# Optimization experiments

Hardware: AMD Instinct MI355X
Metric: run time of the kernel (lower is better)

## Reference

```python
import jax, jax.numpy as jnp
import numpy as np

DIM = 1024
FF = 4096
BATCH = 4
SEQ = 2048
EPS = 1e-5


def setup_inputs() -> dict:
    key = jax.random.key(0)
    ks = jax.random.split(key, 8)
    x = jax.random.normal(ks[0], (BATCH, SEQ, DIM), dtype=jnp.float32)
    # phazor init: exp(2j*pi*arange(dim)/dim) * |randn(dim)|
    ang = 2.0 * np.pi * jnp.arange(DIM, dtype=jnp.float32) / DIM
    mag = jnp.abs(jax.random.normal(ks[1], (DIM,), dtype=jnp.float32))
    phazor_re = mag * jnp.cos(ang)
    phazor_im = mag * jnp.sin(ang)
    last_re = jax.random.normal(ks[2], (DIM,), dtype=jnp.float32)
    last_im = jax.random.normal(ks[3], (DIM,), dtype=jnp.float32)
    w1 = jax.random.normal(ks[4], (FF, DIM), dtype=jnp.float32) * DIM ** -0.5
    b1 = jnp.zeros((FF,), dtype=jnp.float32)
    w2 = jax.random.normal(ks[5], (DIM, FF), dtype=jnp.float32) * FF ** -0.5
    b2 = jnp.zeros((DIM,), dtype=jnp.float32)
    return {
        'x': x,
        'ln1_w': jnp.ones((DIM,), jnp.float32), 'ln1_b': jnp.zeros((DIM,), jnp.float32),
        'ln2_w': jnp.ones((DIM,), jnp.float32), 'ln2_b': jnp.zeros((DIM,), jnp.float32),
        'sc_lin': jnp.ones((DIM,), jnp.float32),
        'phazor_re': phazor_re, 'phazor_im': phazor_im,
        'last_re': last_re, 'last_im': last_im,
        'w1': w1, 'b1': b1, 'w2': w2, 'b2': b2,
    }


def _layer_norm(x, w, b):
    mu = jnp.mean(x, axis=-1, keepdims=True)
    var = jnp.mean(jnp.square(x - mu), axis=-1, keepdims=True)
    return (x - mu) * jax.lax.rsqrt(var + EPS) * w + b


def _sconv(x, phazor_re, phazor_im, last_re, last_im):
    B, L, D = x.shape
    dtype = x.dtype
    xc = x.astype(jnp.complex64)
    p_raw = phazor_re + 1j * phazor_im
    # tanh(|p|) * exp(i*angle(p))
    p = (jnp.tanh(jnp.abs(p_raw)) * jnp.exp(1j * jnp.angle(p_raw))).astype(jnp.complex64)
    t = jnp.arange(L)[:, None]
    prog = jnp.power(p[None, :], t)            # [L, D] complex
    filt_fft = jnp.fft.fft(prog, n=2 * L, axis=0)   # [2L, D]
    x_fft = jnp.fft.fft(xc, n=2 * L, axis=1)        # [B, 2L, D]
    conv = jnp.fft.ifft(filt_fft[None] * x_fft, axis=1)[:, :L]  # [B, L, D]
    last = (last_re + 1j * last_im)[None, None, :]  # [1,1,D] broadcast over batch
    conv_with_past = conv + last * prog[None] * p[None, None]
    return conv_with_past.real.astype(dtype)


def reference(x, ln1_w, ln1_b, ln2_w, ln2_b, sc_lin,
              phazor_re, phazor_im, last_re, last_im,
              w1, b1, w2, b2):
    # SConv branch
    x_res = x
    h = _layer_norm(x, ln1_w, ln1_b)
    h = jax.nn.silu(h)
    h = _sconv(h, phazor_re, phazor_im, last_re, last_im)
    h = h * sc_lin
    x = h + x_res
    # FFN branch
    x_res = x
    h = _layer_norm(x, ln2_w, ln2_b)
    h = jax.nn.silu(jnp.einsum('bld,fd->blf', h, w1) + b1)
    h = jnp.einsum('blf,df->bld', h, w2) + b2
    return h + x_res
```

## Files before the change

kernel.cpp:

```cpp
#include <hip/hip_runtime.h>
#include <cmath>


#define DIMD 1024
#define FFD  4096
#define BATCH 4
#define SEQL 2048
#define MROWS (BATCH*SEQL)
#define EPSF 1e-5f
#define CHUNKS 128
#define CLEN (SEQL/CHUNKS)

typedef __attribute__((ext_vector_type(8))) _Float16 half8;
typedef __attribute__((ext_vector_type(4))) _Float16 half4;
typedef __attribute__((ext_vector_type(4))) float    floatx4;

#define E_OFF    0u
#define SV_OFF   4194304u
#define H2_OFF   8388608u
#define W1H_OFF  25165824u
#define W2H_OFF  33554432u
#define Y1_OFF   41943040u

__device__ __forceinline__ void load_lds16(const _Float16* g, _Float16* l) {
    __builtin_amdgcn_global_load_lds(
        (const __attribute__((address_space(1))) unsigned int*)g,
        (__attribute__((address_space(3))) unsigned int*)l,
        16, 0, 0);
}

__device__ __forceinline__ void wave_reduce2(float& s, float& q) {
    #pragma unroll
    for (int off = 32; off; off >>= 1) {
        s += __shfl_down(s, off, 64);
        q += __shfl_down(q, off, 64);
    }
}

__device__ __forceinline__ void get_p(const float* pre, const float* pim, int d,
                                      float& pr, float& pi) {
    float re = pre[d], im = pim[d];
    float r = sqrtf(re * re + im * im);
    float t = tanhf(r) / fmaxf(r, 1e-30f);
    pr = re * t; pi = im * t;
}

__global__ __launch_bounds__(256)
void cast2_f32_f16(const float* __restrict__ w1, const float* __restrict__ w2,
                   _Float16* __restrict__ o1, _Float16* __restrict__ o2) {
    int i = (blockIdx.x * 256 + threadIdx.x) * 4;
    const float* src = w1;
    _Float16* dst = o1;
    if (i >= FFD * DIMD) { i -= FFD * DIMD; src = w2; dst = o2; }
    float4 v = *(const float4*)(src + i);
    half4 o;
    o.x = (_Float16)v.x; o.y = (_Float16)v.y; o.z = (_Float16)v.z; o.w = (_Float16)v.w;
    *(half4*)(dst + i) = o;
}

__global__ __launch_bounds__(256)
void scan_phase1(const float* __restrict__ x, const float* __restrict__ lw,
                 const float* __restrict__ lb, const float* __restrict__ pre,
                 const float* __restrict__ pim, float2* __restrict__ e) {
    const int tid = threadIdx.x;
    const int d0 = tid * 4;
    const int c = blockIdx.x, bb = blockIdx.y;
    const int lane = tid & 63, wave = tid >> 6;
    __shared__ float2 red[2][4];

    float pr[4], pi[4], sr[4] = {}, si[4] = {};
    #pragma unroll
    for (int q = 0; q < 4; ++q) get_p(pre, pim, d0 + q, pr[q], pi[q]);
    const float4 wv = *(const float4*)(lw + d0);
    const float4 bv = *(const float4*)(lb + d0);
    const size_t rowbase = ((size_t)bb * SEQL + (size_t)c * CLEN) * DIMD;

    for (int j = 0; j < CLEN; ++j) {
        float4 v = *(const float4*)(x + rowbase + (size_t)j * DIMD + d0);
        float s = (v.x + v.y) + (v.z + v.w);
        float q2 = (v.x * v.x + v.y * v.y) + (v.z * v.z + v.w * v.w);
        wave_reduce2(s, q2);
        if (lane == 0) red[j & 1][wave] = make_float2(s, q2);
        __syncthreads();
        float2 r0 = red[j & 1][0], r1 = red[j & 1][1];
        float2 r2 = red[j & 1][2], r3 = red[j & 1][3];
        s = (r0.x + r1.x) + (r2.x + r3.x);
        q2 = (r0.y + r1.y) + (r2.y + r3.y);
        const float mu = s * (1.f / DIMD);
        const float rs = rsqrtf(q2 * (1.f / DIMD) - mu * mu + EPSF);
        float o[4] = {
            (v.x - mu) * rs * wv.x + bv.x, (v.y - mu) * rs * wv.y + bv.y,
            (v.z - mu) * rs * wv.z + bv.z, (v.w - mu) * rs * wv.w + bv.w };
        #pragma unroll
        for (int q = 0; q < 4; ++q) {
            float hv = o[q] / (1.f + __expf(-o[q]));
            float nr = pr[q] * sr[q] - pi[q] * si[q] + hv;
            float ni = pr[q] * si[q] + pi[q] * sr[q];
            sr[q] = nr; si[q] = ni;
        }
    }
    float2* ep = e + ((size_t)bb * CHUNKS + c) * DIMD + d0;
    #pragma unroll
    for (int q = 0; q < 4; ++q) ep[q] = make_float2(sr[q], si[q]);
}

__global__ __launch_bounds__(256)
void scan_combine(const float2* __restrict__ e, const float* __restrict__ pre,
                  const float* __restrict__ pim, const float* __restrict__ lre,
                  const float* __restrict__ lim, float2* __restrict__ sv) {
    const int d = blockIdx.x * 256 + threadIdx.x;
    const int bb = blockIdx.y;
    float pr, pi; get_p(pre, pim, d, pr, pi);
    float qr = pr, qi = pi;
    #pragma unroll
    for (int s = 0; s < 4; ++s) {
        float nr = qr * qr - qi * qi;
        float ni = 2.f * qr * qi;
        qr = nr; qi = ni;
    }
    float sr = lre[d], si = lim[d];
    #pragma unroll 4
    for (int c = 0; c < CHUNKS; ++c) {
        const size_t idx = ((size_t)bb * CHUNKS + c) * DIMD + d;
        sv[idx] = make_float2(sr, si);
        float2 ec = e[idx];
        float nr = qr * sr - qi * si + ec.x;
        float ni = qr * si + qi * sr + ec.y;
        sr = nr; si = ni;
    }
}

__global__ __launch_bounds__(256)
void scan_phase2(const float* __restrict__ x, const float* __restrict__ l1w,
                 const float* __restrict__ l1b, const float* __restrict__ l2w,
                 const float* __restrict__ l2b, const float* __restrict__ pre,
                 const float* __restrict__ pim, const float* __restrict__ sc,
                 const float2* __restrict__ sv, float* __restrict__ x2,
                 _Float16* __restrict__ h2) {
    const int tid = threadIdx.x;
    const int d0 = tid * 4;
    const int c = blockIdx.x, bb = blockIdx.y;
    const int lane = tid & 63, wave = tid >> 6;
    __shared__ float2 redA[2][4];
    __shared__ float2 redB[2][4];

    float pr[4], pi[4], sr[4], si[4];
    #pragma unroll
    for (int q = 0; q < 4; ++q) {
        get_p(pre, pim, d0 + q, pr[q], pi[q]);
        float2 s0 = sv[((size_t)bb * CHUNKS + c) * DIMD + d0 + q];
        sr[q] = s0.x; si[q] = s0.y;
    }
    const float4 w1v = *(const float4*)(l1w + d0);
    const float4 b1v = *(const float4*)(l1b + d0);
    const float4 w2v = *(const float4*)(l2w + d0);
    const float4 b2v = *(const float4*)(l2b + d0);
    const float4 scv = *(const float4*)(sc + d0);
    const size_t rowbase = ((size_t)bb * SEQL + (size_t)c * CLEN) * DIMD;

    for (int j = 0; j < CLEN; ++j) {
        float4 v = *(const float4*)(x + rowbase + (size_t)j * DIMD + d0);
        float s = (v.x + v.y) + (v.z + v.w);
        float q2 = (v.x * v.x + v.y * v.y) + (v.z * v.z + v.w * v.w);
        wave_reduce2(s, q2);
        if (lane == 0) redA[j & 1][wave] = make_float2(s, q2);
        __syncthreads();
        {
            float2 r0 = redA[j & 1][0], r1 = redA[j & 1][1];
            float2 r2 = redA[j & 1][2], r3 = redA[j & 1][3];
            s = (r0.x + r1.x) + (r2.x + r3.x);
            q2 = (r0.y + r1.y) + (r2.y + r3.y);
        }
        const float mu = s * (1.f / DIMD);
        const float rs = rsqrtf(q2 * (1.f / DIMD) - mu * mu + EPSF);
        float o[4] = {
            (v.x - mu) * rs * w1v.x + b1v.x, (v.y - mu) * rs * w1v.y + b1v.y,
            (v.z - mu) * rs * w1v.z + b1v.z, (v.w - mu) * rs * w1v.w + b1v.w };
        #pragma unroll
        for (int q = 0; q < 4; ++q) {
            float hv = o[q] / (1.f + __expf(-o[q]));
            float nr = pr[q] * sr[q] - pi[q] * si[q] + hv;
            float ni = pr[q] * si[q] + pi[q] * sr[q];
            sr[q] = nr; si[q] = ni;
        }
        float4 xv;
        xv.x = v.x + scv.x * sr[0];
        xv.y = v.y + scv.y * sr[1];
        xv.z = v.z + scv.z * sr[2];
        xv.w = v.w + scv.w * sr[3];
        *(float4*)(x2 + rowbase + (size_t)j * DIMD + d0) = xv;
        float s2 = (xv.x + xv.y) + (xv.z + xv.w);
        float q3 = (xv.x * xv.x + xv.y * xv.y) + (xv.z * xv.z + xv.w * xv.w);
        wave_reduce2(s2, q3);
        if (lane == 0) redB[j & 1][wave] = make_float2(s2, q3);
        __syncthreads();
        {
            float2 r0 = redB[j & 1][0], r1 = redB[j & 1][1];
            float2 r2 = redB[j & 1][2], r3 = redB[j & 1][3];
            s2 = (r0.x + r1.x) + (r2.x + r3.x);
            q3 = (r0.y + r1.y) + (r2.y + r3.y);
        }
        const float mu2 = s2 * (1.f / DIMD);
        const float rs2 = rsqrtf(q3 * (1.f / DIMD) - mu2 * mu2 + EPSF);
        half4 hh;
        hh.x = (_Float16)((xv.x - mu2) * rs2 * w2v.x + b2v.x);
        hh.y = (_Float16)((xv.y - mu2) * rs2 * w2v.y + b2v.y);
        hh.z = (_Float16)((xv.z - mu2) * rs2 * w2v.z + b2v.z);
        hh.w = (_Float16)((xv.w - mu2) * rs2 * w2v.w + b2v.w);
        *(half4*)(h2 + rowbase + (size_t)j * DIMD + d0) = hh;
    }
}

#define BM 128
#define BN 128
#define BK 64

__global__ __launch_bounds__(256)
void gemm_bt(const _Float16* __restrict__ A, const _Float16* __restrict__ W,
             const float* __restrict__ bias, _Float16* __restrict__ out_h,
             const float* resid, float* out_f, int N, int K, int epi) {
    __shared__ _Float16 As[BM * BK];
    __shared__ _Float16 Bs[BN * BK];
    const int tid  = threadIdx.x;
    const int lane = tid & 63;
    const int wave = tid >> 6;
    const int wm = (wave >> 1) * 64;
    const int wn = (wave & 1) * 64;
    const size_t m0 = (size_t)blockIdx.y * BM;
    const size_t n0 = (size_t)blockIdx.x * BN;
    const int fr = lane & 15;
    const int quad = lane >> 4;

    const int srow = wave * 32 + (lane >> 3);
    const int ccp  = ((lane & 7) ^ (lane >> 3)) * 8;
    const _Float16* ag = A + (m0 + srow) * (size_t)K + ccp;
    const _Float16* wg = W + (n0 + srow) * (size_t)K + ccp;
    _Float16* asl = &As[(wave * 32) * BK];
    _Float16* bsl = &Bs[(wave * 32) * BK];

    floatx4 acc[4][4] = {};

    for (int k0 = 0; k0 < K; k0 += BK) {
        #pragma unroll
        for (int t = 0; t < 4; ++t) {
            load_lds16(ag + k0 + (size_t)(t * 8) * K, asl + t * 8 * BK);
            load_lds16(wg + k0 + (size_t)(t * 8) * K, bsl + t * 8 * BK);
        }
        __syncthreads();
        #pragma unroll
        for (int kk = 0; kk < BK; kk += 32) {
            half8 af[4], bf[4];
            #pragma unroll
            for (int i = 0; i < 4; ++i) {
                const int slot = (((kk >> 3) + quad) ^ (fr & 7)) * 8;
                af[i] = *(const half8*)(&As[(wm + i * 16 + fr) * BK + slot]);
                bf[i] = *(const half8*)(&Bs[(wn + i * 16 + fr) * BK + slot]);
            }
            #pragma unroll
            for (int i = 0; i < 4; ++i)
                #pragma unroll
                for (int j = 0; j < 4; ++j)
                    acc[i][j] = __builtin_amdgcn_mfma_f32_16x16x32_f16(
                        af[i], bf[j], acc[i][j], 0, 0, 0);
        }
        __syncthreads();
    }

    #pragma unroll
    for (int i = 0; i < 4; ++i) {
        #pragma unroll
        for (int j = 0; j < 4; ++j) {
            #pragma unroll
            for (int r = 0; r < 4; ++r) {
                const size_t gm = m0 + wm + i * 16 + quad * 4 + r;
                const size_t gn = n0 + wn + j * 16 + fr;
                float v = acc[i][j][r] + bias[gn];
                if (epi == 1) {
                    float sl = v / (1.f + __expf(-v));
                    out_h[gm * N + gn] = (_Float16)sl;
                } else {
                    out_f[gm * N + gn] = v + resid[gm * N + gn];
                }
            }
        }
    }
}

extern "C" void kernel_launch(void* const* d_in, const int* in_sizes, int n_in,
                              void* d_out, int out_size, void* d_ws, size_t ws_size,
                              hipStream_t stream) {
    const float* x    = (const float*)d_in[0];
    const float* ln1w = (const float*)d_in[1];
    const float* ln1b = (const float*)d_in[2];
    const float* ln2w = (const float*)d_in[3];
    const float* ln2b = (const float*)d_in[4];
    const float* sc   = (const float*)d_in[5];
    const float* pre  = (const float*)d_in[6];
    const float* pim  = (const float*)d_in[7];
    const float* lre  = (const float*)d_in[8];
    const float* lim  = (const float*)d_in[9];
    const float* w1   = (const float*)d_in[10];
    const float* b1   = (const float*)d_in[11];
    const float* w2   = (const float*)d_in[12];
    const float* b2   = (const float*)d_in[13];

    char* ws = (char*)d_ws;
    float2*     e   = (float2*)(ws + E_OFF);
    float2*     sv  = (float2*)(ws + SV_OFF);
    _Float16*   h2  = (_Float16*)(ws + H2_OFF);
    _Float16*   w1h = (_Float16*)(ws + W1H_OFF);
    _Float16*   w2h = (_Float16*)(ws + W2H_OFF);
    _Float16*   y1  = (_Float16*)(ws + Y1_OFF);
    float*      x2  = (float*)d_out;
    float*      outp = (float*)d_out;

    cast2_f32_f16<<<dim3(2 * FFD * DIMD / 1024), 256, 0, stream>>>(w1, w2, w1h, w2h);
    scan_phase1<<<dim3(CHUNKS, BATCH), 256, 0, stream>>>(x, ln1w, ln1b, pre, pim, e);
    scan_combine<<<dim3(DIMD / 256, BATCH), 256, 0, stream>>>(e, pre, pim, lre, lim, sv);
    scan_phase2<<<dim3(CHUNKS, BATCH), 256, 0, stream>>>(
        x, ln1w, ln1b, ln2w, ln2b, pre, pim, sc, sv, x2, h2);
    gemm_bt<<<dim3(FFD / BN, MROWS / BM), 256, 0, stream>>>(
        h2, w1h, b1, y1, nullptr, nullptr, FFD, DIMD, 1);
    gemm_bt<<<dim3(DIMD / BN, MROWS / BM), 256, 0, stream>>>(
        y1, w2h, b2, nullptr, x2, outp, DIMD, FFD, 2);
}
```

Baseline: 395.7 us.

## Preload chunk rows into registers and batch layernorm reductions with single barrier

Doubles the number of scan chunks so each block handles 8 rows, loads all rows of a chunk into registers up front, and computes every row's layernorm statistics before a single barrier instead of one barrier per row. The second layernorm in phase 2 is likewise batched behind one barrier. The combine step's chunk power and workspace offsets are updated for the new chunk length. This cuts per-row barrier latency and exposes memory-level parallelism, at the cost of more registers, a longer serial combine over 256 chunks, and a larger carry workspace.

Measured after the change: 393.2 us. About the same (-0.6%).

```diff
diff --git a/kernel.cpp b/kernel.cpp
--- a/kernel.cpp
+++ b/kernel.cpp
@@ -8,7 +8,7 @@
 #define SEQL 2048
 #define MROWS (BATCH*SEQL)
 #define EPSF 1e-5f
-#define CHUNKS 128
+#define CHUNKS 256
 #define CLEN (SEQL/CHUNKS)
 
 typedef __attribute__((ext_vector_type(8))) _Float16 half8;
@@ -16,11 +16,11 @@
 typedef __attribute__((ext_vector_type(4))) float    floatx4;
 
 #define E_OFF    0u
-#define SV_OFF   4194304u
-#define H2_OFF   8388608u
-#define W1H_OFF  25165824u
-#define W2H_OFF  33554432u
-#define Y1_OFF   41943040u
+#define SV_OFF   8388608u
+#define H2_OFF   16777216u
+#define W1H_OFF  33554432u
+#define W2H_OFF  41943040u
+#define Y1_OFF   50331648u
 
 __device__ __forceinline__ void load_lds16(const _Float16* g, _Float16* l) {
     __builtin_amdgcn_global_load_lds(
@@ -66,31 +66,40 @@
     const int d0 = tid * 4;
     const int c = blockIdx.x, bb = blockIdx.y;
     const int lane = tid & 63, wave = tid >> 6;
-    __shared__ float2 red[2][4];
+    __shared__ float2 red[CLEN][4];
+
+    const size_t rowbase = ((size_t)bb * SEQL + (size_t)c * CLEN) * DIMD;
+    float4 xv[CLEN];
+    #pragma unroll
+    for (int j = 0; j < CLEN; ++j)
+        xv[j] = *(const float4*)(x + rowbase + (size_t)j * DIMD + d0);
+
+    #pragma unroll
+    for (int j = 0; j < CLEN; ++j) {
+        float s = (xv[j].x + xv[j].y) + (xv[j].z + xv[j].w);
+        float q = (xv[j].x * xv[j].x + xv[j].y * xv[j].y)
+                + (xv[j].z * xv[j].z + xv[j].w * xv[j].w);
+        wave_reduce2(s, q);
+        if (lane == 0) red[j][wave] = make_float2(s, q);
+    }
+    __syncthreads();
 
     float pr[4], pi[4], sr[4] = {}, si[4] = {};
     #pragma unroll
     for (int q = 0; q < 4; ++q) get_p(pre, pim, d0 + q, pr[q], pi[q]);
     const float4 wv = *(const float4*)(lw + d0);
     const float4 bv = *(const float4*)(lb + d0);
-    const size_t rowbase = ((size_t)bb * SEQL + (size_t)c * CLEN) * DIMD;
-
-    for (int j = 0; j < CLEN; ++j) {
-        float4 v = *(const float4*)(x + rowbase + (size_t)j * DIMD + d0);
-        float s = (v.x + v.y) + (v.z + v.w);
-        float q2 = (v.x * v.x + v.y * v.y) + (v.z * v.z + v.w * v.w);
-        wave_reduce2(s, q2);
-        if (lane == 0) red[j & 1][wave] = make_float2(s, q2);
-        __syncthreads();
-        float2 r0 = red[j & 1][0], r1 = red[j & 1][1];
-        float2 r2 = red[j & 1][2], r3 = red[j & 1][3];
-        s = (r0.x + r1.x) + (r2.x + r3.x);
-        q2 = (r0.y + r1.y) + (r2.y + r3.y);
+
+    #pragma unroll
+    for (int j = 0; j < CLEN; ++j) {
+        float2 r0 = red[j][0], r1 = red[j][1], r2 = red[j][2], r3 = red[j][3];
+        float s = (r0.x + r1.x) + (r2.x + r3.x);
+        float q2 = (r0.y + r1.y) + (r2.y + r3.y);
         const float mu = s * (1.f / DIMD);
         const float rs = rsqrtf(q2 * (1.f / DIMD) - mu * mu + EPSF);
         float o[4] = {
-            (v.x - mu) * rs * wv.x + bv.x, (v.y - mu) * rs * wv.y + bv.y,
-            (v.z - mu) * rs * wv.z + bv.z, (v.w - mu) * rs * wv.w + bv.w };
+            (xv[j].x - mu) * rs * wv.x + bv.x, (xv[j].y - mu) * rs * wv.y + bv.y,
+            (xv[j].z - mu) * rs * wv.z + bv.z, (xv[j].w - mu) * rs * wv.w + bv.w };
         #pragma unroll
         for (int q = 0; q < 4; ++q) {
             float hv = o[q] / (1.f + __expf(-o[q]));
@@ -113,13 +122,13 @@
     float pr, pi; get_p(pre, pim, d, pr, pi);
     float qr = pr, qi = pi;
     #pragma unroll
-    for (int s = 0; s < 4; ++s) {
+    for (int s = 0; s < 3; ++s) {
         float nr = qr * qr - qi * qi;
         float ni = 2.f * qr * qi;
         qr = nr; qi = ni;
     }
     float sr = lre[d], si = lim[d];
-    #pragma unroll 4
+    #pragma unroll 8
     for (int c = 0; c < CHUNKS; ++c) {
         const size_t idx = ((size_t)bb * CHUNKS + c) * DIMD + d;
         sv[idx] = make_float2(sr, si);
@@ -141,8 +150,24 @@
     const int d0 = tid * 4;
     const int c = blockIdx.x, bb = blockIdx.y;
     const int lane = tid & 63, wave = tid >> 6;
-    __shared__ float2 redA[2][4];
-    __shared__ float2 redB[2][4];
+    __shared__ float2 redA[CLEN][4];
+    __shared__ float2 redB[CLEN][4];
+
+    const size_t rowbase = ((size_t)bb * SEQL + (size_t)c * CLEN) * DIMD;
+    float4 xv[CLEN];
+    #pragma unroll
+    for (int j = 0; j < CLEN; ++j)
+        xv[j] = *(const float4*)(x + rowbase + (size_t)j * DIMD + d0);
+
+    #pragma unroll
+    for (int j = 0; j < CLEN; ++j) {
+        float s = (xv[j].x + xv[j].y) + (xv[j].z + xv[j].w);
+        float q = (xv[j].x * xv[j].x + xv[j].y * xv[j].y)
+                + (xv[j].z * xv[j].z + xv[j].w * xv[j].w);
+        wave_reduce2(s, q);
+        if (lane == 0) redA[j][wave] = make_float2(s, q);
+    }
+    __syncthreads();
 
     float pr[4], pi[4], sr[4], si[4];
     #pragma unroll
@@ -153,29 +178,18 @@
     }
     const float4 w1v = *(const float4*)(l1w + d0);
     const float4 b1v = *(const float4*)(l1b + d0);
-    const float4 w2v = *(const float4*)(l2w + d0);
-    const float4 b2v = *(const float4*)(l2b + d0);
     const float4 scv = *(const float4*)(sc + d0);
-    const size_t rowbase = ((size_t)bb * SEQL + (size_t)c * CLEN) * DIMD;
-
-    for (int j = 0; j < CLEN; ++j) {
-        float4 v = *(const float4*)(x + rowbase + (size_t)j * DIMD + d0);
-        float s = (v.x + v.y) + (v.z + v.w);
-        float q2 = (v.x * v.x + v.y * v.y) + (v.z * v.z + v.w * v.w);
-        wave_reduce2(s, q2);
-        if (lane == 0) redA[j & 1][wave] = make_float2(s, q2);
-        __syncthreads();
-        {
-            float2 r0 = redA[j & 1][0], r1 = redA[j & 1][1];
-            float2 r2 = redA[j & 1][2], r3 = redA[j & 1][3];
-            s = (r0.x + r1.x) + (r2.x + r3.x);
-            q2 = (r0.y + r1.y) + (r2.y + r3.y);
-        }
+
+    #pragma unroll
+    for (int j = 0; j < CLEN; ++j) {
+        float2 r0 = redA[j][0], r1 = redA[j][1], r2 = redA[j][2], r3 = redA[j][3];
+        float s = (r0.x + r1.x) + (r2.x + r3.x);
+        float q2 = (r0.y + r1.y) + (r2.y + r3.y);
         const float mu = s * (1.f / DIMD);
         const float rs = rsqrtf(q2 * (1.f / DIMD) - mu * mu + EPSF);
         float o[4] = {
-            (v.x - mu) * rs * w1v.x + b1v.x, (v.y - mu) * rs * w1v.y + b1v.y,
-            (v.z - mu) * rs * w1v.z + b1v.z, (v.w - mu) * rs * w1v.w + b1v.w };
+            (xv[j].x - mu) * rs * w1v.x + b1v.x, (xv[j].y - mu) * rs * w1v.y + b1v.y,
+            (xv[j].z - mu) * rs * w1v.z + b1v.z, (xv[j].w - mu) * rs * w1v.w + b1v.w };
         #pragma unroll
         for (int q = 0; q < 4; ++q) {
             float hv = o[q] / (1.f + __expf(-o[q]));
@@ -183,30 +197,37 @@
             float ni = pr[q] * si[q] + pi[q] * sr[q];
             sr[q] = nr; si[q] = ni;
         }
-        float4 xv;
-        xv.x = v.x + scv.x * sr[0];
-        xv.y = v.y + scv.y * sr[1];
-        xv.z = v.z + scv.z * sr[2];
-        xv.w = v.w + scv.w * sr[3];
-        *(float4*)(x2 + rowbase + (size_t)j * DIMD + d0) = xv;
-        float s2 = (xv.x + xv.y) + (xv.z + xv.w);
-        float q3 = (xv.x * xv.x + xv.y * xv.y) + (xv.z * xv.z + xv.w * xv.w);
-        wave_reduce2(s2, q3);
-        if (lane == 0) redB[j & 1][wave] = make_float2(s2, q3);
-        __syncthreads();
-        {
-            float2 r0 = redB[j & 1][0], r1 = redB[j & 1][1];
-            float2 r2 = redB[j & 1][2], r3 = redB[j & 1][3];
-            s2 = (r0.x + r1.x) + (r2.x + r3.x);
-            q3 = (r0.y + r1.y) + (r2.y + r3.y);
-        }
-        const float mu2 = s2 * (1.f / DIMD);
-        const float rs2 = rsqrtf(q3 * (1.f / DIMD) - mu2 * mu2 + EPSF);
+        xv[j].x += scv.x * sr[0];
+        xv[j].y += scv.y * sr[1];
+        xv[j].z += scv.z * sr[2];
+        xv[j].w += scv.w * sr[3];
+        *(float4*)(x2 + rowbase + (size_t)j * DIMD + d0) = xv[j];
+    }
+
+    #pragma unroll
+    for (int j = 0; j < CLEN; ++j) {
+        float s = (xv[j].x + xv[j].y) + (xv[j].z + xv[j].w);
+        float q = (xv[j].x * xv[j].x + xv[j].y * xv[j].y)
+                + (xv[j].z * xv[j].z + xv[j].w * xv[j].w);
+        wave_reduce2(s, q);
+        if (lane == 0) redB[j][wave] = make_float2(s, q);
+    }
+    __syncthreads();
+
+    const float4 w2v = *(const float4*)(l2w + d0);
+    const float4 b2v = *(const float4*)(l2b + d0);
+    #pragma unroll
+    for (int j = 0; j < CLEN; ++j) {
+        float2 r0 = redB[j][0], r1 = redB[j][1], r2 = redB[j][2], r3 = redB[j][3];
+        float s = (r0.x + r1.x) + (r2.x + r3.x);
+        float q2 = (r0.y + r1.y) + (r2.y + r3.y);
+        const float mu = s * (1.f / DIMD);
+        const float rs = rsqrtf(q2 * (1.f / DIMD) - mu * mu + EPSF);
         half4 hh;
-        hh.x = (_Float16)((xv.x - mu2) * rs2 * w2v.x + b2v.x);
-        hh.y = (_Float16)((xv.y - mu2) * rs2 * w2v.y + b2v.y);
-        hh.z = (_Float16)((xv.z - mu2) * rs2 * w2v.z + b2v.z);
-        hh.w = (_Float16)((xv.w - mu2) * rs2 * w2v.w + b2v.w);
+        hh.x = (_Float16)((xv[j].x - mu) * rs * w2v.x + b2v.x);
+        hh.y = (_Float16)((xv[j].y - mu) * rs * w2v.y + b2v.y);
+        hh.z = (_Float16)((xv[j].z - mu) * rs * w2v.z + b2v.z);
+        hh.w = (_Float16)((xv[j].w - mu) * rs * w2v.w + b2v.w);
         *(half4*)(h2 + rowbase + (size_t)j * DIMD + d0) = hh;
     }
 }
```
